# Kernel tuning notes

Hardware: AMD Instinct MI355X
Metric: run time of the kernel (lower is better)

## Reference

```python
import jax, jax.numpy as jnp
import numpy as np

N_NODES = 50000
N_EDGES = 1600000
IN_CH = 128
HID = 64
HEADS = 2
OUT_CH2 = HID // 8  # 8
OUT_FC = 1
N_GRAPHS = 64
NEG_SLOPE = 0.2


def setup_inputs() -> dict:
    key = jax.random.key(0)
    ks = jax.random.split(key, 12)
    x = jax.random.normal(ks[0], (N_NODES, IN_CH), dtype=jnp.float32)
    edge_index = jax.random.randint(ks[1], (2, N_EDGES), 0, N_NODES, dtype=jnp.int32)
    batch = jnp.sort(jax.random.randint(ks[2], (N_NODES,), 0, N_GRAPHS, dtype=jnp.int32))
    s = lambda fan: 1.0 / np.sqrt(fan)
    W1 = jax.random.normal(ks[3], (IN_CH, HEADS * HID), dtype=jnp.float32) * s(IN_CH)
    att_src1 = jax.random.normal(ks[4], (HEADS, HID), dtype=jnp.float32) * s(HID)
    att_dst1 = jax.random.normal(ks[5], (HEADS, HID), dtype=jnp.float32) * s(HID)
    b1 = jnp.zeros((HEADS * HID,), dtype=jnp.float32)
    W2 = jax.random.normal(ks[6], (HEADS * HID, OUT_CH2), dtype=jnp.float32) * s(HEADS * HID)
    att_src2 = jax.random.normal(ks[7], (1, OUT_CH2), dtype=jnp.float32) * s(OUT_CH2)
    att_dst2 = jax.random.normal(ks[8], (1, OUT_CH2), dtype=jnp.float32) * s(OUT_CH2)
    b2 = jnp.zeros((OUT_CH2,), dtype=jnp.float32)
    fcW = jax.random.normal(ks[9], (OUT_CH2, OUT_FC), dtype=jnp.float32) * s(OUT_CH2)
    fcb = jnp.zeros((OUT_FC,), dtype=jnp.float32)
    return {"x": x, "edge_index": edge_index, "batch": batch,
            "W1": W1, "att_src1": att_src1, "att_dst1": att_dst1, "b1": b1,
            "W2": W2, "att_src2": att_src2, "att_dst2": att_dst2, "b2": b2,
            "fcW": fcW, "fcb": fcb}


def gat_conv(x, edge_index, W, att_src, att_dst, bias, heads, out_ch):
    """PyG GATConv (concat=True, add_self_loops=True, negative_slope=0.2, eval mode)."""
    n = x.shape[0]
    loop = jnp.arange(n, dtype=edge_index.dtype)
    src = jnp.concatenate([edge_index[0], loop])
    dst = jnp.concatenate([edge_index[1], loop])
    h = (x @ W).reshape(n, heads, out_ch)                 # [N,H,C]
    a_src = jnp.sum(h * att_src[None], axis=-1)           # [N,H]
    a_dst = jnp.sum(h * att_dst[None], axis=-1)           # [N,H]
    logits = jax.nn.leaky_relu(a_src[src] + a_dst[dst], NEG_SLOPE)  # [E,H]
    m = jax.ops.segment_max(logits, dst, num_segments=n)  # segment softmax over dst
    e = jnp.exp(logits - m[dst])
    denom = jax.ops.segment_sum(e, dst, num_segments=n)
    alpha = e / denom[dst]                                # [E,H]
    msg = h[src] * alpha[:, :, None]                      # [E,H,C]
    out = jax.ops.segment_sum(msg, dst, num_segments=n)   # [N,H,C]
    return out.reshape(n, heads * out_ch) + bias


def reference(x, edge_index, batch, W1, att_src1, att_dst1, b1,
              W2, att_src2, att_dst2, b2, fcW, fcb):
    h = gat_conv(x, edge_index, W1, att_src1, att_dst1, b1, HEADS, HID)
    h = jax.nn.relu(h)
    h = gat_conv(h, edge_index, W2, att_src2, att_dst2, b2, 1, OUT_CH2)
    h = jax.nn.relu(h)
    # global_mean_pool over graphs
    sums = jax.ops.segment_sum(h, batch, num_segments=N_GRAPHS)
    cnts = jax.ops.segment_sum(jnp.ones((h.shape[0],), h.dtype), batch, num_segments=N_GRAPHS)
    pooled = sums / jnp.maximum(cnts, 1.0)[:, None]       # [G, OUT_CH2]
    y = pooled @ fcW + fcb
    y = 2.0 * jax.nn.sigmoid(y) - 1.0
    return y.squeeze(-1)                                  # [G]
```

## Files before the change

kernel.cpp:

```cpp
#include <hip/hip_runtime.h>
#include <math.h>

#define MAXD 96

__device__ __forceinline__ float lrelu(float v){ return v >= 0.f ? v : 0.2f * v; }

__global__ void scanA(const int* __restrict__ deg, int* __restrict__ excl,
                      int* __restrict__ part, int n){
  __shared__ int s[256];
  int t = threadIdx.x;
  int i = blockIdx.x * 256 + t;
  int v = (i < n) ? deg[i] : 0;
  s[t] = v;
  __syncthreads();
  for (int o = 1; o < 256; o <<= 1){
    int tv = (t >= o) ? s[t - o] : 0;
    __syncthreads();
    s[t] += tv;
    __syncthreads();
  }
  if (i < n) excl[i] = s[t] - v;
  if (t == 255) part[blockIdx.x] = s[t];
}

__global__ void scanBC(int* __restrict__ csrOff, const int* __restrict__ part,
                       int n, int ET, int nbl){
  __shared__ int s[256];
  int t = threadIdx.x, b = blockIdx.x;
  int v = (t < nbl) ? part[t] : 0;
  s[t] = v;
  __syncthreads();
  for (int o = 1; o < 256; o <<= 1){
    int tv = (t >= o) ? s[t - o] : 0;
    __syncthreads();
    s[t] += tv;
    __syncthreads();
  }
  int add = (b > 0) ? s[b - 1] : 0;
  int i = b * 256 + t;
  if (i < n) csrOff[i] += add;
  if (i == 0) csrOff[n] = ET;
}

__global__ void scatterK(const int* __restrict__ srcA, const int* __restrict__ dstA, int E, int ET,
                         const int* __restrict__ off, const int* __restrict__ erank,
                         int* __restrict__ csrc){
  int e = blockIdx.x * blockDim.x + threadIdx.x;
  if (e >= ET) return;
  int s, d;
  if (e < E){ s = srcA[e]; d = dstA[e]; } else { s = e - E; d = s; }
  csrc[off[d] + erank[e]] = s;
}

__global__ __launch_bounds__(256, 2) void gemm1cnt(const float* __restrict__ x, const float* __restrict__ W1,
    const float* __restrict__ attS, const float* __restrict__ attD,
    unsigned char* __restrict__ h1q, float* __restrict__ a1sc, float* __restrict__ a1d, int nN,
    const int* __restrict__ dstA, int E, int ET, int* __restrict__ deg, int* __restrict__ erank){
  __shared__ float4 Ws4[128][32];
  __shared__ float4 xs4[32][32];
  int t = threadIdx.x;
  int b = blockIdx.x;
  int g1b = (int)gridDim.x;
  int CH = (ET + g1b - 1) / g1b;
  int eBeg = b * CH;
  int eEnd = eBeg + CH < ET ? eBeg + CH : ET;

  auto edgeWork = [&](){
    for (int e = eBeg + t; e < eEnd; e += 256){
      int d = (e < E) ? dstA[e] : (e - E);
      erank[e] = atomicAdd(&deg[d], 1);
    }
  };

  auto gemmWork = [&](){
    const float4* Wg = reinterpret_cast<const float4*>(W1);
    #pragma unroll
    for (int i = 0; i < 16; ++i){
      int idx = t + i * 256;
      Ws4[idx >> 5][idx & 31] = Wg[idx];
    }
    int n0 = b * 32;
    const float4* xg = reinterpret_cast<const float4*>(x);
    #pragma unroll
    for (int i = 0; i < 4; ++i){
      int idx = t + i * 256;
      int r = idx >> 5, c = idx & 31;
      int gn = n0 + r; if (gn >= nN) gn = nN - 1;
      xs4[r][c ^ (r & 7)] = xg[(size_t)gn * 32 + c];
    }
    __syncthreads();
    int cb = t & 15, nl = t >> 4;
    int cb2 = cb * 2;
    int c0 = cb * 8;
    int sw = nl & 7;
    float4 accA0 = make_float4(0.f,0.f,0.f,0.f), accA1 = accA0;
    float4 accB0 = accA0, accB1 = accA0;
    #pragma unroll 2
    for (int k4 = 0; k4 < 32; ++k4){
      float4 xv0 = xs4[nl][k4 ^ sw];
      float4 xv1 = xs4[nl + 16][k4 ^ sw];
      float xa[4] = {xv0.x, xv0.y, xv0.z, xv0.w};
      float xb[4] = {xv1.x, xv1.y, xv1.z, xv1.w};
      #pragma unroll
      for (int j = 0; j < 4; ++j){
        float4 wA = Ws4[4 * k4 + j][cb2];
        float4 wB = Ws4[4 * k4 + j][cb2 + 1];
        accA0.x = fmaf(xa[j], wA.x, accA0.x);
        accA0.y = fmaf(xa[j], wA.y, accA0.y);
        accA0.z = fmaf(xa[j], wA.z, accA0.z);
        accA0.w = fmaf(xa[j], wA.w, accA0.w);
        accA1.x = fmaf(xa[j], wB.x, accA1.x);
        accA1.y = fmaf(xa[j], wB.y, accA1.y);
        accA1.z = fmaf(xa[j], wB.z, accA1.z);
        accA1.w = fmaf(xa[j], wB.w, accA1.w);
        accB0.x = fmaf(xb[j], wA.x, accB0.x);
        accB0.y = fmaf(xb[j], wA.y, accB0.y);
        accB0.z = fmaf(xb[j], wA.z, accB0.z);
        accB0.w = fmaf(xb[j], wA.w, accB0.w);
        accB1.x = fmaf(xb[j], wB.x, accB1.x);
        accB1.y = fmaf(xb[j], wB.y, accB1.y);
        accB1.z = fmaf(xb[j], wB.z, accB1.z);
        accB1.w = fmaf(xb[j], wB.w, accB1.w);
      }
    }
    float4 as0 = *reinterpret_cast<const float4*>(attS + c0);
    float4 as1 = *reinterpret_cast<const float4*>(attS + c0 + 4);
    float4 ad0 = *reinterpret_cast<const float4*>(attD + c0);
    float4 ad1 = *reinterpret_cast<const float4*>(attD + c0 + 4);
    #pragma unroll
    for (int j = 0; j < 2; ++j){
      int n = n0 + nl + j * 16;
      if (n >= nN) continue;
      float4 h0 = j ? accB0 : accA0;
      float4 h1v = j ? accB1 : accA1;
      float s = h0.x*as0.x + h0.y*as0.y + h0.z*as0.z + h0.w*as0.w
              + h1v.x*as1.x + h1v.y*as1.y + h1v.z*as1.z + h1v.w*as1.w;
      float d = h0.x*ad0.x + h0.y*ad0.y + h0.z*ad0.z + h0.w*ad0.w
              + h1v.x*ad1.x + h1v.y*ad1.y + h1v.z*ad1.z + h1v.w*ad1.w;
      float am = fmaxf(fmaxf(fmaxf(fabsf(h0.x), fabsf(h0.y)), fmaxf(fabsf(h0.z), fabsf(h0.w))),
                       fmaxf(fmaxf(fabsf(h1v.x), fabsf(h1v.y)), fmaxf(fabsf(h1v.z), fabsf(h1v.w))));
      #pragma unroll
      for (int o = 1; o <= 4; o <<= 1){
        s += __shfl_xor(s, o);
        d += __shfl_xor(d, o);
        am = fmaxf(am, __shfl_xor(am, o));
      }
      float scale = am * (1.f / 127.f);
      float qs = am > 0.f ? 127.f / am : 0.f;
      int q0 = __float2int_rn(h0.x * qs),  q1 = __float2int_rn(h0.y * qs);
      int q2 = __float2int_rn(h0.z * qs),  q3 = __float2int_rn(h0.w * qs);
      int q4 = __float2int_rn(h1v.x * qs), q5 = __float2int_rn(h1v.y * qs);
      int q6 = __float2int_rn(h1v.z * qs), q7 = __float2int_rn(h1v.w * qs);
      uint2 pk;
      pk.x = (q0 & 255) | ((q1 & 255) << 8) | ((q2 & 255) << 16) | ((q3 & 255) << 24);
      pk.y = (q4 & 255) | ((q5 & 255) << 8) | ((q6 & 255) << 16) | ((q7 & 255) << 24);
      *reinterpret_cast<uint2*>(h1q + (size_t)n * 128 + c0) = pk;
      if ((cb & 7) == 0){
        int head = cb >> 3;
        a1sc[n * 4 + head]     = s;
        a1sc[n * 4 + 2 + head] = scale;
        a1d[n * 2 + head]      = d;
      }
    }
  };

  if (b & 1){ edgeWork(); gemmWork(); }
  else      { gemmWork(); edgeWork(); }
}

__global__ __launch_bounds__(256) void agg1(const int* __restrict__ off, const int* __restrict__ csrc,
    const float* __restrict__ a1sc, const float* __restrict__ a1d,
    const unsigned char* __restrict__ h1q, const float* __restrict__ b1,
    const float* __restrict__ W2, const float* __restrict__ attS2, const float* __restrict__ attD2,
    float* __restrict__ h2, float* __restrict__ a2s, float* __restrict__ a2d, int nN){
  __shared__ float al[4][MAXD][2];
  __shared__ int   sidx[4][MAXD];
  int t = threadIdx.x;
  int w = t >> 6, lane = t & 63;
  int n = blockIdx.x * 4 + w;
  if (n >= nN) return;
  int start = off[n], end = off[n + 1];
  int deg = end - start;
  int degc = deg < MAXD ? deg : MAXD;
  float ad0 = a1d[2 * n], ad1 = a1d[2 * n + 1];
  float ls0 = 0.f, ls1 = 0.f;
  for (int i = lane; i < degc; i += 64){
    int s = csrc[start + i];
    sidx[w][i] = s;
    float4 v = *reinterpret_cast<const float4*>(a1sc + 4 * s);
    float e0 = __expf(lrelu(v.x + ad0));
    float e1 = __expf(lrelu(v.y + ad1));
    al[w][i][0] = e0 * v.z;
    al[w][i][1] = e1 * v.w;
    ls0 += e0; ls1 += e1;
  }
  #pragma unroll
  for (int o = 32; o > 0; o >>= 1){
    ls0 += __shfl_xor(ls0, o);
    ls1 += __shfl_xor(ls1, o);
  }
  float d0 = ls0, d1 = ls1;
  int c4 = (lane & 31) * 4;
  int h = c4 >> 6;
  int sub = lane >> 5;
  float4 acc = make_float4(0.f, 0.f, 0.f, 0.f);
  #pragma unroll 8
  for (int k = 0; k < degc; k += 2){
    int e = k + sub;
    bool ok = e < degc;
    int ee = ok ? e : degc - 1;
    int s = sidx[w][ee];
    float wgt = ok ? al[w][ee][h] : 0.f;
    unsigned v = *reinterpret_cast<const unsigned*>(h1q + (size_t)s * 128 + c4);
    int b0 = (int)(char)(v & 255);
    int b1i = (int)(char)((v >> 8) & 255);
    int b2 = (int)(char)((v >> 16) & 255);
    int b3 = (int)(char)(v >> 24);
    acc.x = fmaf(wgt, (float)b0,  acc.x);
    acc.y = fmaf(wgt, (float)b1i, acc.y);
    acc.z = fmaf(wgt, (float)b2,  acc.z);
    acc.w = fmaf(wgt, (float)b3,  acc.w);
  }
  acc.x += __shfl_xor(acc.x, 32);
  acc.y += __shfl_xor(acc.y, 32);
  acc.z += __shfl_xor(acc.z, 32);
  acc.w += __shfl_xor(acc.w, 32);
  float inv = 1.f / (h ? d1 : d0);
  float4 bb = *reinterpret_cast<const float4*>(b1 + c4);
  float oj[4];
  oj[0] = fmaxf(fmaf(acc.x, inv, bb.x), 0.f);
  oj[1] = fmaxf(fmaf(acc.y, inv, bb.y), 0.f);
  oj[2] = fmaxf(fmaf(acc.z, inv, bb.z), 0.f);
  oj[3] = fmaxf(fmaf(acc.w, inv, bb.w), 0.f);
  const float4* W2v = reinterpret_cast<const float4*>(W2);
  float p8[8] = {0.f,0.f,0.f,0.f,0.f,0.f,0.f,0.f};
  #pragma unroll
  for (int j = 0; j < 4; ++j){
    float4 wlo = W2v[(c4 + j) * 2];
    float4 whi = W2v[(c4 + j) * 2 + 1];
    p8[0] = fmaf(oj[j], wlo.x, p8[0]); p8[1] = fmaf(oj[j], wlo.y, p8[1]);
    p8[2] = fmaf(oj[j], wlo.z, p8[2]); p8[3] = fmaf(oj[j], wlo.w, p8[3]);
    p8[4] = fmaf(oj[j], whi.x, p8[4]); p8[5] = fmaf(oj[j], whi.y, p8[5]);
    p8[6] = fmaf(oj[j], whi.z, p8[6]); p8[7] = fmaf(oj[j], whi.w, p8[7]);
  }
  #pragma unroll
  for (int o = 16; o > 0; o >>= 1){
    #pragma unroll
    for (int cc = 0; cc < 8; ++cc) p8[cc] += __shfl_xor(p8[cc], o);
  }
  if (lane == 0){
    *reinterpret_cast<float4*>(h2 + (size_t)n * 8)     = make_float4(p8[0], p8[1], p8[2], p8[3]);
    *reinterpret_cast<float4*>(h2 + (size_t)n * 8 + 4) = make_float4(p8[4], p8[5], p8[6], p8[7]);
    float s2 = 0.f, dd2 = 0.f;
    #pragma unroll
    for (int cc = 0; cc < 8; ++cc){
      s2  = fmaf(p8[cc], attS2[cc], s2);
      dd2 = fmaf(p8[cc], attD2[cc], dd2);
    }
    a2s[n] = s2; a2d[n] = dd2;
  }
}

__global__ __launch_bounds__(256) void agg2(const int* __restrict__ off, const int* __restrict__ csrc,
    const float* __restrict__ a2s, const float* __restrict__ a2d,
    const float* __restrict__ h2, const float* __restrict__ b2, float* __restrict__ out2, int nN){
  __shared__ float al[4][MAXD];
  __shared__ int sidx[4][MAXD];
  int t = threadIdx.x;
  int w = t >> 6, lane = t & 63;
  int n = blockIdx.x * 4 + w;
  if (n >= nN) return;
  int start = off[n], end = off[n + 1];
  int deg = end - start, degc = deg < MAXD ? deg : MAXD;
  float ad = a2d[n];
  float ls = 0.f;
  for (int i = lane; i < degc; i += 64){
    int s = csrc[start + i];
    sidx[w][i] = s;
    float e = __expf(lrelu(a2s[s] + ad));
    al[w][i] = e;
    ls += e;
  }
  #pragma unroll
  for (int o = 32; o > 0; o >>= 1) ls += __shfl_xor(ls, o);
  float dv = ls;
  int c = lane & 7, eb = lane >> 3;
  float acc = 0.f;
  #pragma unroll 4
  for (int k = 0; k < degc; k += 8){
    int e = k + eb;
    bool ok = e < degc;
    int ee = ok ? e : degc - 1;
    float wgt = ok ? al[w][ee] : 0.f;
    acc = fmaf(wgt, h2[(size_t)sidx[w][ee] * 8 + c], acc);
  }
  acc += __shfl_xor(acc, 8);
  acc += __shfl_xor(acc, 16);
  acc += __shfl_xor(acc, 32);
  if (lane < 8) out2[(size_t)n * 8 + lane] = fmaxf(acc / dv + b2[lane], 0.f);
}

__global__ __launch_bounds__(256) void poolFC(const float* __restrict__ out2,
    const int* __restrict__ batch, const float* __restrict__ fcW,
    const float* __restrict__ fcb, float* __restrict__ out, int nN){
  __shared__ float red[256];
  int g = blockIdx.x;
  int lo = 0, hi = nN;
  while (lo < hi){ int m = (lo + hi) >> 1; if (batch[m] < g) lo = m + 1; else hi = m; }
  int s = lo;
  hi = nN;
  while (lo < hi){ int m = (lo + hi) >> 1; if (batch[m] < g + 1) lo = m + 1; else hi = m; }
  int e = lo;
  int t = threadIdx.x;
  int c = t & 7, row = t >> 3;
  float acc = 0.f;
  for (int i = s + row; i < e; i += 32) acc += out2[(size_t)i * 8 + c];
  red[t] = acc;
  __syncthreads();
  for (int o = 128; o >= 8; o >>= 1){
    if (t < o) red[t] += red[t + o];
    __syncthreads();
  }
  if (t == 0){
    float cc = fmaxf((float)(e - s), 1.0f);
    float y = fcb[0];
    #pragma unroll
    for (int c2 = 0; c2 < 8; ++c2) y += (red[c2] / cc) * fcW[c2];
    out[g] = 2.f / (1.f + expf(-y)) - 1.f;
  }
}

extern "C" void kernel_launch(void* const* d_in, const int* in_sizes, int n_in,
                              void* d_out, int out_size, void* d_ws, size_t ws_size,
                              hipStream_t stream){
  const float* x    = (const float*)d_in[0];
  const int*   ei   = (const int*)d_in[1];
  const int*   batch= (const int*)d_in[2];
  const float* W1   = (const float*)d_in[3];
  const float* aS1  = (const float*)d_in[4];
  const float* aD1  = (const float*)d_in[5];
  const float* b1   = (const float*)d_in[6];
  const float* W2   = (const float*)d_in[7];
  const float* aS2  = (const float*)d_in[8];
  const float* aD2  = (const float*)d_in[9];
  const float* b2   = (const float*)d_in[10];
  const float* fcW  = (const float*)d_in[11];
  const float* fcb  = (const float*)d_in[12];
  float* out = (float*)d_out;

  const int N  = in_sizes[0] / 128;
  const int E  = in_sizes[1] / 2;
  const int ET = E + N;
  const int G  = 64;

  const int* eiSrc = ei;
  const int* eiDst = ei + E;

  char* w = (char*)d_ws;
  size_t o = 0;
  auto alloc = [&](size_t bytes)->char*{
    o = (o + 255) & ~(size_t)255;
    char* p = w + o;
    o += bytes;
    return p;
  };
  int*   deg    = (int*)  alloc((size_t)N * 4);
  size_t zbytes = (size_t)N * 4;
  int*   csrOff = (int*)  alloc((size_t)(N + 1) * 4);
  int*   part   = (int*)  alloc(256 * 4);
  int*   erank  = (int*)  alloc((size_t)ET * 4);
  int*   csrc   = (int*)  alloc((size_t)ET * 4);
  unsigned char* h1q = (unsigned char*)alloc((size_t)N * 128);
  float* a1sc   = (float*)alloc((size_t)N * 4 * 4);
  float* a1d    = (float*)alloc((size_t)N * 2 * 4);
  float* h2     = (float*)alloc((size_t)N * 8 * 4);
  float* a2s    = (float*)alloc((size_t)N * 4);
  float* a2d    = (float*)alloc((size_t)N * 4);
  float* out2   = (float*)alloc((size_t)N * 8 * 4);
  (void)ws_size; (void)n_in; (void)out_size;

  hipMemsetAsync(deg, 0, zbytes, stream);

  int ebl = (ET + 255) / 256;
  int nbl = (N + 255) / 256;
  int g1b = (N + 31) / 32;

  gemm1cnt<<<g1b, 256, 0, stream>>>(x, W1, aS1, aD1, h1q, a1sc, a1d, N,
                                    eiDst, E, ET, deg, erank);
  scanA   <<<nbl, 256, 0, stream>>>(deg, csrOff, part, N);
  scanBC  <<<nbl, 256, 0, stream>>>(csrOff, part, N, ET, nbl);
  scatterK<<<ebl, 256, 0, stream>>>(eiSrc, eiDst, E, ET, csrOff, erank, csrc);

  agg1 <<<(N + 3) / 4, 256, 0, stream>>>(csrOff, csrc, a1sc, a1d, h1q, b1, W2, aS2, aD2, h2, a2s, a2d, N);
  agg2 <<<(N + 3) / 4, 256, 0, stream>>>(csrOff, csrc, a2s, a2d, h2, b2, out2, N);
  poolFC<<<G, 256, 0, stream>>>(out2, batch, fcW, fcb, out, N);
}
```

Measured before the change: 222.4 us.

## Split layer-1 aggregation per head into two passes over half-width feature tables

The int8 layer-1 features are stored as two separate per-head tables of 64 bytes per node. Aggregation is split into two kernels, one per head, so each pass gathers from a 3.2 MB table that fits better in cache. The first head's normalized result goes through an intermediate bf16 buffer that the second kernel reads back before applying W2. The cost is an extra kernel launch, the CSR indices and attention logits being read twice, more bf16 rounding, and extra global traffic for the intermediate.

```diff
diff --git a/kernel.cpp b/kernel.cpp
--- a/kernel.cpp
+++ b/kernel.cpp
@@ -4,6 +4,11 @@
 #define MAXD 96
 
 __device__ __forceinline__ float lrelu(float v){ return v >= 0.f ? v : 0.2f * v; }
+
+__device__ __forceinline__ unsigned short f2bf(float f){
+  unsigned u = __float_as_uint(f);
+  return (unsigned short)((u + 0x7fffu + ((u >> 16) & 1u)) >> 16);
+}
 
 __global__ void scanA(const int* __restrict__ deg, int* __restrict__ excl,
                       int* __restrict__ part, int n){
@@ -54,7 +59,8 @@
 
 __global__ __launch_bounds__(256, 2) void gemm1cnt(const float* __restrict__ x, const float* __restrict__ W1,
     const float* __restrict__ attS, const float* __restrict__ attD,
-    unsigned char* __restrict__ h1q, float* __restrict__ a1sc, float* __restrict__ a1d, int nN,
+    unsigned char* __restrict__ h1q0, unsigned char* __restrict__ h1q1,
+    float* __restrict__ a1sc, float* __restrict__ a1d, int nN,
     const int* __restrict__ dstA, int E, int ET, int* __restrict__ deg, int* __restrict__ erank){
   __shared__ float4 Ws4[128][32];
   __shared__ float4 xs4[32][32];
@@ -154,7 +160,9 @@
       uint2 pk;
       pk.x = (q0 & 255) | ((q1 & 255) << 8) | ((q2 & 255) << 16) | ((q3 & 255) << 24);
       pk.y = (q4 & 255) | ((q5 & 255) << 8) | ((q6 & 255) << 16) | ((q7 & 255) << 24);
-      *reinterpret_cast<uint2*>(h1q + (size_t)n * 128 + c0) = pk;
+      unsigned char* dstp = (c0 < 64) ? (h1q0 + (size_t)n * 64 + c0)
+                                      : (h1q1 + (size_t)n * 64 + (c0 - 64));
+      *reinterpret_cast<uint2*>(dstp) = pk;
       if ((cb & 7) == 0){
         int head = cb >> 3;
         a1sc[n * 4 + head]     = s;
@@ -168,12 +176,10 @@
   else      { gemmWork(); edgeWork(); }
 }
 
-__global__ __launch_bounds__(256) void agg1(const int* __restrict__ off, const int* __restrict__ csrc,
+__global__ __launch_bounds__(256) void agg1a(const int* __restrict__ off, const int* __restrict__ csrc,
     const float* __restrict__ a1sc, const float* __restrict__ a1d,
-    const unsigned char* __restrict__ h1q, const float* __restrict__ b1,
-    const float* __restrict__ W2, const float* __restrict__ attS2, const float* __restrict__ attD2,
-    float* __restrict__ h2, float* __restrict__ a2s, float* __restrict__ a2d, int nN){
-  __shared__ float al[4][MAXD][2];
+    const unsigned char* __restrict__ h1q0, unsigned short* __restrict__ out1h0, int nN){
+  __shared__ float al[4][MAXD];
   __shared__ int   sidx[4][MAXD];
   int t = threadIdx.x;
   int w = t >> 6, lane = t & 63;
@@ -182,69 +188,128 @@
   int start = off[n], end = off[n + 1];
   int deg = end - start;
   int degc = deg < MAXD ? deg : MAXD;
-  float ad0 = a1d[2 * n], ad1 = a1d[2 * n + 1];
-  float ls0 = 0.f, ls1 = 0.f;
+  float ad0 = a1d[2 * n];
+  float ls0 = 0.f;
   for (int i = lane; i < degc; i += 64){
     int s = csrc[start + i];
     sidx[w][i] = s;
     float4 v = *reinterpret_cast<const float4*>(a1sc + 4 * s);
     float e0 = __expf(lrelu(v.x + ad0));
-    float e1 = __expf(lrelu(v.y + ad1));
-    al[w][i][0] = e0 * v.z;
-    al[w][i][1] = e1 * v.w;
-    ls0 += e0; ls1 += e1;
+    al[w][i] = e0 * v.z;
+    ls0 += e0;
   }
   #pragma unroll
-  for (int o = 32; o > 0; o >>= 1){
-    ls0 += __shfl_xor(ls0, o);
-    ls1 += __shfl_xor(ls1, o);
-  }
-  float d0 = ls0, d1 = ls1;
-  int c4 = (lane & 31) * 4;
-  int h = c4 >> 6;
-  int sub = lane >> 5;
+  for (int o = 32; o > 0; o >>= 1) ls0 += __shfl_xor(ls0, o);
+  float inv = 1.f / ls0;
+  int c4 = (lane & 15) * 4;
+  int eb = lane >> 4;
   float4 acc = make_float4(0.f, 0.f, 0.f, 0.f);
   #pragma unroll 8
-  for (int k = 0; k < degc; k += 2){
-    int e = k + sub;
+  for (int k = 0; k < degc; k += 4){
+    int e = k + eb;
     bool ok = e < degc;
     int ee = ok ? e : degc - 1;
     int s = sidx[w][ee];
-    float wgt = ok ? al[w][ee][h] : 0.f;
-    unsigned v = *reinterpret_cast<const unsigned*>(h1q + (size_t)s * 128 + c4);
-    int b0 = (int)(char)(v & 255);
-    int b1i = (int)(char)((v >> 8) & 255);
-    int b2 = (int)(char)((v >> 16) & 255);
-    int b3 = (int)(char)(v >> 24);
-    acc.x = fmaf(wgt, (float)b0,  acc.x);
-    acc.y = fmaf(wgt, (float)b1i, acc.y);
-    acc.z = fmaf(wgt, (float)b2,  acc.z);
-    acc.w = fmaf(wgt, (float)b3,  acc.w);
-  }
-  acc.x += __shfl_xor(acc.x, 32);
-  acc.y += __shfl_xor(acc.y, 32);
-  acc.z += __shfl_xor(acc.z, 32);
-  acc.w += __shfl_xor(acc.w, 32);
-  float inv = 1.f / (h ? d1 : d0);
-  float4 bb = *reinterpret_cast<const float4*>(b1 + c4);
-  float oj[4];
-  oj[0] = fmaxf(fmaf(acc.x, inv, bb.x), 0.f);
-  oj[1] = fmaxf(fmaf(acc.y, inv, bb.y), 0.f);
-  oj[2] = fmaxf(fmaf(acc.z, inv, bb.z), 0.f);
-  oj[3] = fmaxf(fmaf(acc.w, inv, bb.w), 0.f);
+    float wgt = ok ? al[w][ee] : 0.f;
+    unsigned v = *reinterpret_cast<const unsigned*>(h1q0 + (size_t)s * 64 + c4);
+    acc.x = fmaf(wgt, (float)(char)(v & 255),         acc.x);
+    acc.y = fmaf(wgt, (float)(char)((v >> 8) & 255),  acc.y);
+    acc.z = fmaf(wgt, (float)(char)((v >> 16) & 255), acc.z);
+    acc.w = fmaf(wgt, (float)(char)(v >> 24),         acc.w);
+  }
+  acc.x += __shfl_xor(acc.x, 16); acc.x += __shfl_xor(acc.x, 32);
+  acc.y += __shfl_xor(acc.y, 16); acc.y += __shfl_xor(acc.y, 32);
+  acc.z += __shfl_xor(acc.z, 16); acc.z += __shfl_xor(acc.z, 32);
+  acc.w += __shfl_xor(acc.w, 16); acc.w += __shfl_xor(acc.w, 32);
+  if (lane < 16){
+    uint2 pk;
+    pk.x = (unsigned)f2bf(acc.x * inv) | ((unsigned)f2bf(acc.y * inv) << 16);
+    pk.y = (unsigned)f2bf(acc.z * inv) | ((unsigned)f2bf(acc.w * inv) << 16);
+    *reinterpret_cast<uint2*>(out1h0 + (size_t)n * 64 + c4) = pk;
+  }
+}
+
+__global__ __launch_bounds__(256) void agg1b(const int* __restrict__ off, const int* __restrict__ csrc,
+    const float* __restrict__ a1sc, const float* __restrict__ a1d,
+    const unsigned char* __restrict__ h1q1, const unsigned short* __restrict__ out1h0,
+    const float* __restrict__ b1, const float* __restrict__ W2,
+    const float* __restrict__ attS2, const float* __restrict__ attD2,
+    float* __restrict__ h2, float* __restrict__ a2s, float* __restrict__ a2d, int nN){
+  __shared__ float al[4][MAXD];
+  __shared__ int   sidx[4][MAXD];
+  int t = threadIdx.x;
+  int w = t >> 6, lane = t & 63;
+  int n = blockIdx.x * 4 + w;
+  if (n >= nN) return;
+  int start = off[n], end = off[n + 1];
+  int deg = end - start;
+  int degc = deg < MAXD ? deg : MAXD;
+  float ad1 = a1d[2 * n + 1];
+  float ls1 = 0.f;
+  for (int i = lane; i < degc; i += 64){
+    int s = csrc[start + i];
+    sidx[w][i] = s;
+    float4 v = *reinterpret_cast<const float4*>(a1sc + 4 * s);
+    float e1 = __expf(lrelu(v.y + ad1));
+    al[w][i] = e1 * v.w;
+    ls1 += e1;
+  }
+  #pragma unroll
+  for (int o = 32; o > 0; o >>= 1) ls1 += __shfl_xor(ls1, o);
+  float inv = 1.f / ls1;
+  int l = lane & 15;
+  int c4 = l * 4;
+  int eb = lane >> 4;
+  float4 acc = make_float4(0.f, 0.f, 0.f, 0.f);
+  #pragma unroll 8
+  for (int k = 0; k < degc; k += 4){
+    int e = k + eb;
+    bool ok = e < degc;
+    int ee = ok ? e : degc - 1;
+    int s = sidx[w][ee];
+    float wgt = ok ? al[w][ee] : 0.f;
+    unsigned v = *reinterpret_cast<const unsigned*>(h1q1 + (size_t)s * 64 + c4);
+    acc.x = fmaf(wgt, (float)(char)(v & 255),         acc.x);
+    acc.y = fmaf(wgt, (float)(char)((v >> 8) & 255),  acc.y);
+    acc.z = fmaf(wgt, (float)(char)((v >> 16) & 255), acc.z);
+    acc.w = fmaf(wgt, (float)(char)(v >> 24),         acc.w);
+  }
+  acc.x += __shfl_xor(acc.x, 16); acc.x += __shfl_xor(acc.x, 32);
+  acc.y += __shfl_xor(acc.y, 16); acc.y += __shfl_xor(acc.y, 32);
+  acc.z += __shfl_xor(acc.z, 16); acc.z += __shfl_xor(acc.z, 32);
+  acc.w += __shfl_xor(acc.w, 16); acc.w += __shfl_xor(acc.w, 32);
+  float avg1[4] = {acc.x * inv, acc.y * inv, acc.z * inv, acc.w * inv};
+  uint2 pk0 = *reinterpret_cast<const uint2*>(out1h0 + (size_t)n * 64 + c4);
+  float a0[4];
+  a0[0] = __uint_as_float(pk0.x << 16);
+  a0[1] = __uint_as_float(pk0.x & 0xffff0000u);
+  a0[2] = __uint_as_float(pk0.y << 16);
+  a0[3] = __uint_as_float(pk0.y & 0xffff0000u);
+  float4 b_lo = *reinterpret_cast<const float4*>(b1 + c4);
+  float4 b_hi = *reinterpret_cast<const float4*>(b1 + 64 + c4);
+  float bj0[4] = {b_lo.x, b_lo.y, b_lo.z, b_lo.w};
+  float bj1[4] = {b_hi.x, b_hi.y, b_hi.z, b_hi.w};
   const float4* W2v = reinterpret_cast<const float4*>(W2);
   float p8[8] = {0.f,0.f,0.f,0.f,0.f,0.f,0.f,0.f};
   #pragma unroll
   for (int j = 0; j < 4; ++j){
-    float4 wlo = W2v[(c4 + j) * 2];
-    float4 whi = W2v[(c4 + j) * 2 + 1];
-    p8[0] = fmaf(oj[j], wlo.x, p8[0]); p8[1] = fmaf(oj[j], wlo.y, p8[1]);
-    p8[2] = fmaf(oj[j], wlo.z, p8[2]); p8[3] = fmaf(oj[j], wlo.w, p8[3]);
-    p8[4] = fmaf(oj[j], whi.x, p8[4]); p8[5] = fmaf(oj[j], whi.y, p8[5]);
-    p8[6] = fmaf(oj[j], whi.z, p8[6]); p8[7] = fmaf(oj[j], whi.w, p8[7]);
+    float o0 = fmaxf(a0[j] + bj0[j], 0.f);
+    float o1 = fmaxf(avg1[j] + bj1[j], 0.f);
+    float4 w0lo = W2v[(c4 + j) * 2];
+    float4 w0hi = W2v[(c4 + j) * 2 + 1];
+    float4 w1lo = W2v[(64 + c4 + j) * 2];
+    float4 w1hi = W2v[(64 + c4 + j) * 2 + 1];
+    p8[0] = fmaf(o0, w0lo.x, fmaf(o1, w1lo.x, p8[0]));
+    p8[1] = fmaf(o0, w0lo.y, fmaf(o1, w1lo.y, p8[1]));
+    p8[2] = fmaf(o0, w0lo.z, fmaf(o1, w1lo.z, p8[2]));
+    p8[3] = fmaf(o0, w0lo.w, fmaf(o1, w1lo.w, p8[3]));
+    p8[4] = fmaf(o0, w0hi.x, fmaf(o1, w1hi.x, p8[4]));
+    p8[5] = fmaf(o0, w0hi.y, fmaf(o1, w1hi.y, p8[5]));
+    p8[6] = fmaf(o0, w0hi.z, fmaf(o1, w1hi.z, p8[6]));
+    p8[7] = fmaf(o0, w0hi.w, fmaf(o1, w1hi.w, p8[7]));
   }
   #pragma unroll
-  for (int o = 16; o > 0; o >>= 1){
+  for (int o = 8; o > 0; o >>= 1){
     #pragma unroll
     for (int cc = 0; cc < 8; ++cc) p8[cc] += __shfl_xor(p8[cc], o);
   }
@@ -370,7 +435,9 @@
   int*   part   = (int*)  alloc(256 * 4);
   int*   erank  = (int*)  alloc((size_t)ET * 4);
   int*   csrc   = (int*)  alloc((size_t)ET * 4);
-  unsigned char* h1q = (unsigned char*)alloc((size_t)N * 128);
+  unsigned char* h1q0 = (unsigned char*)alloc((size_t)N * 64);
+  unsigned char* h1q1 = (unsigned char*)alloc((size_t)N * 64);
+  unsigned short* out1h0 = (unsigned short*)alloc((size_t)N * 64 * 2);
   float* a1sc   = (float*)alloc((size_t)N * 4 * 4);
   float* a1d    = (float*)alloc((size_t)N * 2 * 4);
   float* h2     = (float*)alloc((size_t)N * 8 * 4);
@@ -385,13 +452,15 @@
   int nbl = (N + 255) / 256;
   int g1b = (N + 31) / 32;
 
-  gemm1cnt<<<g1b, 256, 0, stream>>>(x, W1, aS1, aD1, h1q, a1sc, a1d, N,
+  gemm1cnt<<<g1b, 256, 0, stream>>>(x, W1, aS1, aD1, h1q0, h1q1, a1sc, a1d, N,
                                     eiDst, E, ET, deg, erank);
   scanA   <<<nbl, 256, 0, stream>>>(deg, csrOff, part, N);
   scanBC  <<<nbl, 256, 0, stream>>>(csrOff, part, N, ET, nbl);
   scatterK<<<ebl, 256, 0, stream>>>(eiSrc, eiDst, E, ET, csrOff, erank, csrc);
 
-  agg1 <<<(N + 3) / 4, 256, 0, stream>>>(csrOff, csrc, a1sc, a1d, h1q, b1, W2, aS2, aD2, h2, a2s, a2d, N);
+  agg1a<<<(N + 3) / 4, 256, 0, stream>>>(csrOff, csrc, a1sc, a1d, h1q0, out1h0, N);
+  agg1b<<<(N + 3) / 4, 256, 0, stream>>>(csrOff, csrc, a1sc, a1d, h1q1, out1h0,
+                                         b1, W2, aS2, aD2, h2, a2s, a2d, N);
   agg2 <<<(N + 3) / 4, 256, 0, stream>>>(csrOff, csrc, a2s, a2d, h2, b2, out2, N);
   poolFC<<<G, 256, 0, stream>>>(out2, batch, fcW, fcb, out, N);
 }
```

Result: slower. 284.7 us (+28.0%).
